# Kernel optimization log

Hardware: AMD Instinct MI355X
Metric: run time of the kernel (lower is better)

The kernel has to match this reference:

```python
import jax, jax.numpy as jnp
import numpy as np

B, T, C, H = 256, 256, 1024, 64

def setup_inputs() -> dict:
    key = jax.random.key(0)
    kx, kk, kq, kv = jax.random.split(key, 4)
    x = jax.random.normal(kx, (B, T, C), dtype=jnp.float32)
    # Dense kernels init'd with normal(stddev=0.02), stored as [in, out] like flax
    Wk = jax.random.normal(kk, (C, H), dtype=jnp.float32) * 0.02
    Wq = jax.random.normal(kq, (C, H), dtype=jnp.float32) * 0.02
    Wv = jax.random.normal(kv, (C, H), dtype=jnp.float32) * 0.02
    return {"x": x, "Wk": Wk, "Wq": Wq, "Wv": Wv}

def reference(x, Wk, Wq, Wv):
    # single-head causal self-attention (eval mode: dropout is identity)
    k = jnp.einsum('btc,ch->bth', x, Wk)      # [B,T,H]
    q = jnp.einsum('btc,ch->bth', x, Wq)      # [B,T,H]
    v = jnp.einsum('btc,ch->bth', x, Wv)      # [B,T,H]
    scale = jnp.asarray(k.shape[-1], k.dtype) ** -0.5
    wei = jnp.einsum('bth,bsh->bts', q, k) * scale  # [B,T,T]
    t = x.shape[1]
    causal = jnp.tril(jnp.ones((t, t), dtype=bool))
    wei = jnp.where(causal, wei, -jnp.inf)
    wei = jax.nn.softmax(wei, axis=-1)
    out = jnp.einsum('bts,bsh->bth', wei, v)  # [B,T,H]
    return out
```

## Files before the change

kernel.cpp:

```cpp
#include <hip/hip_runtime.h>

typedef float f32x4 __attribute__((ext_vector_type(4)));
typedef short s16x8 __attribute__((ext_vector_type(8)));

#define MFMA16 __builtin_amdgcn_mfma_f32_16x16x32_bf16

__device__ __forceinline__ unsigned short f2bf(float f) {
    union { float f; unsigned u; } v; v.f = f;
    unsigned r = v.u + 0x7FFF + ((v.u >> 16) & 1);
    return (unsigned short)(r >> 16);
}

__global__ void prep_w(const float* __restrict__ Wk, const float* __restrict__ Wq,
                       const float* __restrict__ Wv, unsigned short* __restrict__ wt) {
    int n = blockIdx.x;
    int tid = threadIdx.x;
    const float* src; int col; float sc = 1.0f;
    if (n < 64)       { src = Wq; col = n;       sc = 0.125f; }
    else if (n < 128) { src = Wk; col = n - 64; }
    else              { src = Wv; col = n - 128; }
#pragma unroll
    for (int i = 0; i < 4; i++) {
        int c = i * 256 + tid;
        wt[n * 1024 + c] = f2bf(src[c * 64 + col] * sc);
    }
}

__global__ __launch_bounds__(512, 2) void fused_kernel(const float* __restrict__ x,
                                                       const unsigned short* __restrict__ wt,
                                                       float* __restrict__ out) {
    __shared__ unsigned short Ql[256 * 72];
    __shared__ unsigned short Kl[256 * 72];
    __shared__ unsigned short Vt[64 * 264];
    __shared__ unsigned short Pl[8][16 * 56];

    const int tid  = threadIdx.x;
    const int lane = tid & 63;
    const int wid  = tid >> 6;
    const int quad = lane >> 4;
    const int l15  = lane & 15;
    const int b    = blockIdx.x;
    const int m0   = wid * 32;

    const float* xb = x + (long)b * 256 * 1024;

    f32x4 acc[2][12] = {};

    const float* arow0 = xb + (long)(m0 + l15) * 1024 + quad * 8;
    const float* arow1 = arow0 + 16 * 1024;
    const unsigned short* wrow = wt + (long)l15 * 1024 + quad * 8;

    float4 pa0 = *(const float4*)(arow0);
    float4 pa1 = *(const float4*)(arow0 + 4);
    float4 pa2 = *(const float4*)(arow1);
    float4 pa3 = *(const float4*)(arow1 + 4);

    for (int k0 = 0; k0 < 1024; k0 += 32) {
        s16x8 bf[12];
#pragma unroll
        for (int nt = 0; nt < 12; nt++)
            bf[nt] = *(const s16x8*)(wrow + (long)nt * 16 * 1024 + k0);

        s16x8 af0 = { (short)f2bf(pa0.x), (short)f2bf(pa0.y), (short)f2bf(pa0.z), (short)f2bf(pa0.w),
                      (short)f2bf(pa1.x), (short)f2bf(pa1.y), (short)f2bf(pa1.z), (short)f2bf(pa1.w) };
        s16x8 af1 = { (short)f2bf(pa2.x), (short)f2bf(pa2.y), (short)f2bf(pa2.z), (short)f2bf(pa2.w),
                      (short)f2bf(pa3.x), (short)f2bf(pa3.y), (short)f2bf(pa3.z), (short)f2bf(pa3.w) };

        const int kn = (k0 + 32 < 1024) ? k0 + 32 : 0;
        pa0 = *(const float4*)(arow0 + kn);
        pa1 = *(const float4*)(arow0 + kn + 4);
        pa2 = *(const float4*)(arow1 + kn);
        pa3 = *(const float4*)(arow1 + kn + 4);

#pragma unroll
        for (int nt = 0; nt < 12; nt++) {
            acc[0][nt] = MFMA16(af0, bf[nt], acc[0][nt], 0, 0, 0);
            acc[1][nt] = MFMA16(af1, bf[nt], acc[1][nt], 0, 0, 0);
        }
    }

#pragma unroll
    for (int mt = 0; mt < 2; mt++) {
#pragma unroll
        for (int nt = 0; nt < 12; nt++) {
            if (nt < 4) {
#pragma unroll
                for (int r = 0; r < 4; r++)
                    Ql[(m0 + mt * 16 + quad * 4 + r) * 72 + nt * 16 + l15] = f2bf(acc[mt][nt][r]);
            } else if (nt < 8) {
#pragma unroll
                for (int r = 0; r < 4; r++)
                    Kl[(m0 + mt * 16 + quad * 4 + r) * 72 + (nt - 4) * 16 + l15] = f2bf(acc[mt][nt][r]);
            } else {
                ushort4 pv;
                pv.x = f2bf(acc[mt][nt][0]); pv.y = f2bf(acc[mt][nt][1]);
                pv.z = f2bf(acc[mt][nt][2]); pv.w = f2bf(acc[mt][nt][3]);
                *(ushort4*)&Vt[((nt - 8) * 16 + l15) * 264 + m0 + mt * 16 + quad * 4] = pv;
            }
        }
    }
    __syncthreads();

    unsigned short* Pw = &Pl[wid][0];

#pragma unroll
    for (int ti = 0; ti < 2; ti++) {
        const int r0 = (ti == 0 ? wid : 15 - wid) * 16;

        s16x8 qf0 = *(const s16x8*)&Ql[(r0 + l15) * 72 + quad * 8];
        s16x8 qf1 = *(const s16x8*)&Ql[(r0 + l15) * 72 + 32 + quad * 8];

        f32x4 o[4] = {};
        float mr[4], lr[4];
#pragma unroll
        for (int r = 0; r < 4; r++) { mr[r] = -1e30f; lr[r] = 0.0f; }

        const int nst = (r0 >> 5) + 1;
        for (int st = 0; st < nst; st++) {
            const int s0 = st * 32;
            s16x8 kf00 = *(const s16x8*)&Kl[(s0 + l15) * 72 + quad * 8];
            s16x8 kf01 = *(const s16x8*)&Kl[(s0 + l15) * 72 + 32 + quad * 8];
            s16x8 kf10 = *(const s16x8*)&Kl[(s0 + 16 + l15) * 72 + quad * 8];
            s16x8 kf11 = *(const s16x8*)&Kl[(s0 + 16 + l15) * 72 + 32 + quad * 8];
            s16x8 vf[4];
#pragma unroll
            for (int n = 0; n < 4; n++)
                vf[n] = *(const s16x8*)&Vt[(n * 16 + l15) * 264 + s0 + quad * 8];

            f32x4 S0 = {0.f, 0.f, 0.f, 0.f}, S1 = {0.f, 0.f, 0.f, 0.f};
            S0 = MFMA16(qf0, kf00, S0, 0, 0, 0);
            S0 = MFMA16(qf1, kf01, S0, 0, 0, 0);
            S1 = MFMA16(qf0, kf10, S1, 0, 0, 0);
            S1 = MFMA16(qf1, kf11, S1, 0, 0, 0);

            if (s0 + 31 > r0) {
#pragma unroll
                for (int r = 0; r < 4; r++) {
                    int t = r0 + quad * 4 + r;
                    if (s0 + l15 > t)      S0[r] = -1e30f;
                    if (s0 + 16 + l15 > t) S1[r] = -1e30f;
                }
            }

            float a4[4];
#pragma unroll
            for (int r = 0; r < 4; r++) {
                float rm = fmaxf(S0[r], S1[r]);
                rm = fmaxf(rm, __shfl_xor(rm, 1));
                rm = fmaxf(rm, __shfl_xor(rm, 2));
                rm = fmaxf(rm, __shfl_xor(rm, 4));
                rm = fmaxf(rm, __shfl_xor(rm, 8));
                float mn = fmaxf(mr[r], rm);
                float al = exp2f((mr[r] - mn) * 1.44269504f);
                mr[r] = mn;
                float p0 = exp2f((S0[r] - mn) * 1.44269504f);
                float p1 = exp2f((S1[r] - mn) * 1.44269504f);
                float rs = p0 + p1;
                rs += __shfl_xor(rs, 1);
                rs += __shfl_xor(rs, 2);
                rs += __shfl_xor(rs, 4);
                rs += __shfl_xor(rs, 8);
                lr[r] = al * lr[r] + rs;
                a4[r] = al;
                Pw[(quad * 4 + r) * 56 + l15]      = f2bf(p0);
                Pw[(quad * 4 + r) * 56 + l15 + 16] = f2bf(p1);
            }
#pragma unroll
            for (int n = 0; n < 4; n++) {
                f32x4 t = o[n];
#pragma unroll
                for (int r = 0; r < 4; r++) t[r] *= a4[r];
                o[n] = t;
            }
            s16x8 pf = *(const s16x8*)&Pw[l15 * 56 + quad * 8];
#pragma unroll
            for (int n = 0; n < 4; n++)
                o[n] = MFMA16(pf, vf[n], o[n], 0, 0, 0);
        }

        float inv[4];
#pragma unroll
        for (int r = 0; r < 4; r++) inv[r] = 1.0f / lr[r];
#pragma unroll
        for (int n = 0; n < 4; n++)
#pragma unroll
            for (int r = 0; r < 4; r++) {
                long t = (long)b * 256 + r0 + quad * 4 + r;
                out[t * 64 + n * 16 + l15] = o[n][r] * inv[r];
            }
    }
}

extern "C" void kernel_launch(void* const* d_in, const int* in_sizes, int n_in,
                              void* d_out, int out_size, void* d_ws, size_t ws_size,
                              hipStream_t stream) {
    const float* x  = (const float*)d_in[0];
    const float* Wk = (const float*)d_in[1];
    const float* Wq = (const float*)d_in[2];
    const float* Wv = (const float*)d_in[3];
    float* out = (float*)d_out;

    unsigned short* wt = (unsigned short*)d_ws;

    prep_w<<<192, 256, 0, stream>>>(Wk, Wq, Wv, wt);
    fused_kernel<<<256, 512, 0, stream>>>(x, wt, out);
}
```

Measured before the change: 476.5 us.

## Stage projection weights in LDS via direct global-to-LDS loads with swizzle

The QKV projection loop now copies 64-wide K-slices of the bf16 weight matrix into shared memory with global_load_lds and an XOR swizzle. Before, every wave read its own copy of the weights straight from global memory. The weight buffer reuses the Q/K shared region. The x loads now cover 64 columns per step, and each step has two barriers. This cuts redundant global and L2 weight traffic across the 8 waves, but adds barrier stalls and drops the old register prefetch of x, so x load latency is less hidden.

```diff
diff --git a/kernel.cpp b/kernel.cpp
--- a/kernel.cpp
+++ b/kernel.cpp
@@ -4,6 +4,9 @@
 typedef short s16x8 __attribute__((ext_vector_type(8)));
 
 #define MFMA16 __builtin_amdgcn_mfma_f32_16x16x32_bf16
+
+typedef const __attribute__((address_space(1))) void* gptr_t;
+typedef __attribute__((address_space(3))) void* lptr_t;
 
 __device__ __forceinline__ unsigned short f2bf(float f) {
     union { float f; unsigned u; } v; v.f = f;
@@ -29,10 +32,12 @@
 __global__ __launch_bounds__(512, 2) void fused_kernel(const float* __restrict__ x,
                                                        const unsigned short* __restrict__ wt,
                                                        float* __restrict__ out) {
-    __shared__ unsigned short Ql[256 * 72];
-    __shared__ unsigned short Kl[256 * 72];
-    __shared__ unsigned short Vt[64 * 264];
-    __shared__ unsigned short Pl[8][16 * 56];
+    __shared__ unsigned short smem[2 * 256 * 72 + 64 * 264 + 8 * 16 * 56];
+    unsigned short* Ql  = smem;
+    unsigned short* Kl  = smem + 256 * 72;
+    unsigned short* Vt  = smem + 2 * 256 * 72;
+    unsigned short* Pl8 = smem + 2 * 256 * 72 + 64 * 264;
+    unsigned short* Wl  = smem;
 
     const int tid  = threadIdx.x;
     const int lane = tid & 63;
@@ -42,42 +47,65 @@
     const int b    = blockIdx.x;
     const int m0   = wid * 32;
 
-    const float* xb = x + (long)b * 256 * 1024;
+    const float* xb  = x + (long)b * 256 * 1024;
+    const float* ar0 = xb + (long)(m0 + l15) * 1024 + quad * 8;
+    const float* ar1 = ar0 + 16 * 1024;
+
+    const int srow = wid * 24 + (lane >> 3);
+    const int cswz = (lane & 7) ^ (srow & 7);
+
+    const unsigned short* wbase0 = Wl + l15 * 64 + ((0 + quad) ^ (l15 & 7)) * 8;
+    const unsigned short* wbase1 = Wl + l15 * 64 + ((4 + quad) ^ (l15 & 7)) * 8;
 
     f32x4 acc[2][12] = {};
 
-    const float* arow0 = xb + (long)(m0 + l15) * 1024 + quad * 8;
-    const float* arow1 = arow0 + 16 * 1024;
-    const unsigned short* wrow = wt + (long)l15 * 1024 + quad * 8;
-
-    float4 pa0 = *(const float4*)(arow0);
-    float4 pa1 = *(const float4*)(arow0 + 4);
-    float4 pa2 = *(const float4*)(arow1);
-    float4 pa3 = *(const float4*)(arow1 + 4);
-
-    for (int k0 = 0; k0 < 1024; k0 += 32) {
-        s16x8 bf[12];
-#pragma unroll
-        for (int nt = 0; nt < 12; nt++)
-            bf[nt] = *(const s16x8*)(wrow + (long)nt * 16 * 1024 + k0);
-
-        s16x8 af0 = { (short)f2bf(pa0.x), (short)f2bf(pa0.y), (short)f2bf(pa0.z), (short)f2bf(pa0.w),
-                      (short)f2bf(pa1.x), (short)f2bf(pa1.y), (short)f2bf(pa1.z), (short)f2bf(pa1.w) };
-        s16x8 af1 = { (short)f2bf(pa2.x), (short)f2bf(pa2.y), (short)f2bf(pa2.z), (short)f2bf(pa2.w),
-                      (short)f2bf(pa3.x), (short)f2bf(pa3.y), (short)f2bf(pa3.z), (short)f2bf(pa3.w) };
-
-        const int kn = (k0 + 32 < 1024) ? k0 + 32 : 0;
-        pa0 = *(const float4*)(arow0 + kn);
-        pa1 = *(const float4*)(arow0 + kn + 4);
-        pa2 = *(const float4*)(arow1 + kn);
-        pa3 = *(const float4*)(arow1 + kn + 4);
-
-#pragma unroll
-        for (int nt = 0; nt < 12; nt++) {
-            acc[0][nt] = MFMA16(af0, bf[nt], acc[0][nt], 0, 0, 0);
-            acc[1][nt] = MFMA16(af1, bf[nt], acc[1][nt], 0, 0, 0);
-        }
-    }
+    for (int t = 0; t < 16; t++) {
+        const int k0 = t * 64;
+        if (t) __syncthreads();
+#pragma unroll
+        for (int j = 0; j < 3; j++) {
+            const unsigned short* src = wt + (long)(srow + j * 8) * 1024 + k0 + cswz * 8;
+            unsigned short* dst = Wl + (wid * 24 + j * 8) * 64;
+            __builtin_amdgcn_global_load_lds((gptr_t)src, (lptr_t)dst, 16, 0, 0);
+        }
+        float4 px0 = *(const float4*)(ar0 + k0);
+        float4 px1 = *(const float4*)(ar0 + k0 + 4);
+        float4 px2 = *(const float4*)(ar0 + k0 + 32);
+        float4 px3 = *(const float4*)(ar0 + k0 + 36);
+        float4 px4 = *(const float4*)(ar1 + k0);
+        float4 px5 = *(const float4*)(ar1 + k0 + 4);
+        float4 px6 = *(const float4*)(ar1 + k0 + 32);
+        float4 px7 = *(const float4*)(ar1 + k0 + 36);
+        __syncthreads();
+
+#pragma unroll
+        for (int kk = 0; kk < 64; kk += 32) {
+            s16x8 bfv[12];
+            const unsigned short* wb = (kk == 0) ? wbase0 : wbase1;
+#pragma unroll
+            for (int nt = 0; nt < 12; nt++)
+                bfv[nt] = *(const s16x8*)(wb + nt * 1024);
+
+            s16x8 af0, af1;
+            if (kk == 0) {
+                af0 = s16x8{ (short)f2bf(px0.x), (short)f2bf(px0.y), (short)f2bf(px0.z), (short)f2bf(px0.w),
+                             (short)f2bf(px1.x), (short)f2bf(px1.y), (short)f2bf(px1.z), (short)f2bf(px1.w) };
+                af1 = s16x8{ (short)f2bf(px4.x), (short)f2bf(px4.y), (short)f2bf(px4.z), (short)f2bf(px4.w),
+                             (short)f2bf(px5.x), (short)f2bf(px5.y), (short)f2bf(px5.z), (short)f2bf(px5.w) };
+            } else {
+                af0 = s16x8{ (short)f2bf(px2.x), (short)f2bf(px2.y), (short)f2bf(px2.z), (short)f2bf(px2.w),
+                             (short)f2bf(px3.x), (short)f2bf(px3.y), (short)f2bf(px3.z), (short)f2bf(px3.w) };
+                af1 = s16x8{ (short)f2bf(px6.x), (short)f2bf(px6.y), (short)f2bf(px6.z), (short)f2bf(px6.w),
+                             (short)f2bf(px7.x), (short)f2bf(px7.y), (short)f2bf(px7.z), (short)f2bf(px7.w) };
+            }
+#pragma unroll
+            for (int nt = 0; nt < 12; nt++) {
+                acc[0][nt] = MFMA16(af0, bfv[nt], acc[0][nt], 0, 0, 0);
+                acc[1][nt] = MFMA16(af1, bfv[nt], acc[1][nt], 0, 0, 0);
+            }
+        }
+    }
+    __syncthreads();
 
 #pragma unroll
     for (int mt = 0; mt < 2; mt++) {
@@ -101,7 +129,7 @@
     }
     __syncthreads();
 
-    unsigned short* Pw = &Pl[wid][0];
+    unsigned short* Pw = Pl8 + wid * (16 * 56);
 
 #pragma unroll
     for (int ti = 0; ti < 2; ti++) {
@@ -167,10 +195,10 @@
             }
 #pragma unroll
             for (int n = 0; n < 4; n++) {
-                f32x4 t = o[n];
-#pragma unroll
-                for (int r = 0; r < 4; r++) t[r] *= a4[r];
-                o[n] = t;
+                f32x4 tt = o[n];
+#pragma unroll
+                for (int r = 0; r < 4; r++) tt[r] *= a4[r];
+                o[n] = tt;
             }
             s16x8 pf = *(const s16x8*)&Pw[l15 * 56 + quad * 8];
 #pragma unroll
```

Measured after the change: 409.4 us. 1.16x faster.
